# Kernel tuning notes

Hardware: AMD Instinct MI355X
Metric: run time of the kernel (lower is better)

## Reference

```python
import jax, jax.numpy as jnp
import numpy as np

D_MODEL = 768
N_HEADS = 12
HEAD_DIM = D_MODEL // N_HEADS
D_FF = 3072
LN_EPS = 1e-12


def layer_norm(x, gamma, beta, eps=LN_EPS):
    mu = jnp.mean(x, axis=-1, keepdims=True)
    var = jnp.var(x, axis=-1, keepdims=True)
    return (x - mu) * jax.lax.rsqrt(var + eps) * gamma + beta


def setup_inputs() -> dict:
    key = jax.random.key(0)
    ks = jax.random.split(key, 16)
    B, S = 4, 2048
    p = lambda k, shape: (jax.random.normal(k, shape, dtype=jnp.float32) * 0.02)
    return {
        "hidden_states": jax.random.normal(ks[0], (B, S, D_MODEL), dtype=jnp.float32),
        "Wq": p(ks[1], (D_MODEL, D_MODEL)), "bq": jnp.zeros((D_MODEL,), jnp.float32),
        "Wk": p(ks[2], (D_MODEL, D_MODEL)), "bk": jnp.zeros((D_MODEL,), jnp.float32),
        "Wv": p(ks[3], (D_MODEL, D_MODEL)), "bv": jnp.zeros((D_MODEL,), jnp.float32),
        "Wo": p(ks[4], (D_MODEL, D_MODEL)), "bo": jnp.zeros((D_MODEL,), jnp.float32),
        "ln1_g": jnp.ones((D_MODEL,), jnp.float32), "ln1_b": jnp.zeros((D_MODEL,), jnp.float32),
        "Wi": p(ks[5], (D_FF, D_MODEL)), "bi": jnp.zeros((D_FF,), jnp.float32),
        "Wf": p(ks[6], (D_MODEL, D_FF)), "bf": jnp.zeros((D_MODEL,), jnp.float32),
        "ln2_g": jnp.ones((D_MODEL,), jnp.float32), "ln2_b": jnp.zeros((D_MODEL,), jnp.float32),
    }


def reference(hidden_states, Wq, bq, Wk, bk, Wv, bv, Wo, bo, ln1_g, ln1_b,
              Wi, bi, Wf, bf, ln2_g, ln2_b):
    B, S, _ = hidden_states.shape
    # Q/K/V projections (computed as in source; outputs then overwritten by constants)
    q = hidden_states @ Wq.T + bq
    k = hidden_states @ Wk.T + bk
    v = hidden_states @ Wv.T + bv
    split = lambda x: x.reshape(B, S, N_HEADS, HEAD_DIM).transpose(0, 2, 1, 3)
    q, k, v = split(q), split(k), split(v)
    # source: torch.full_like(..., 0.01) overwrite of q/k/v
    q = jnp.full_like(q, 0.01)
    k = jnp.full_like(k, 0.01)
    v = jnp.full_like(v, 0.01)
    # naive attention: full [B,H,S,S] score matrix materialized
    scores = jnp.einsum("bhqd,bhkd->bhqk", q, k) / jnp.sqrt(jnp.float32(HEAD_DIM))
    probs = jax.nn.softmax(scores, axis=-1)
    ctx = jnp.einsum("bhqk,bhkd->bhqd", probs, v)
    ctx = ctx.transpose(0, 2, 1, 3).reshape(B, S, D_MODEL)
    # self-output: dense + residual + LayerNorm (dropout is identity in eval)
    attn_out = layer_norm(ctx @ Wo.T + bo + hidden_states, ln1_g, ln1_b)
    # FFN: fc1 + exact GELU, fc2 + residual + LayerNorm
    h = jax.nn.gelu(attn_out @ Wi.T + bi, approximate=False)
    layer_out = layer_norm(h @ Wf.T + bf + attn_out, ln2_g, ln2_b)
    return layer_out
```

## Files before the change

kernel.cpp:

```cpp
#include <hip/hip_runtime.h>
#include <hip/hip_bf16.h>
#include <cstdint>
#include <cstddef>


typedef __bf16 bf16;
typedef __attribute__((ext_vector_type(8))) __bf16 bf16x8;
typedef __attribute__((ext_vector_type(4))) __bf16 bf16x4;
typedef __attribute__((ext_vector_type(16))) float floatx16;

#define DM    768
#define DF    3072
#define MROWS 8192

#define N8          (DF * DM / 8)
#define CONV_BLOCKS (2 * N8 / 256)
#define CVEC_BLOCKS (DM / 4)

__device__ __forceinline__ void gl2lds16(const void* gp, void* lp) {
  __builtin_amdgcn_global_load_lds(
      (__attribute__((address_space(1))) void*)(void*)gp,
      (__attribute__((address_space(3))) void*)lp,
      16, 0, 0);
}

__device__ __forceinline__ float gelu_fast(float x) {
  float x2 = x * x;
  float m  = x * __builtin_fmaf(-0.1029641f, x2, -2.3025851f);
  float e  = __builtin_amdgcn_exp2f(m);
  return x * __builtin_amdgcn_rcpf(1.0f + e);
}

__global__ __launch_bounds__(256)
void prep_kernel(const float* __restrict__ Wi, const float* __restrict__ Wf,
                 bf16* __restrict__ Wib, bf16* __restrict__ Wfb,
                 const float* __restrict__ Wo, const float* __restrict__ bo,
                 float* __restrict__ cvec) {
  if (blockIdx.x < CONV_BLOCKS) {
    int i = blockIdx.x * 256 + threadIdx.x;
    const float* src = (i < N8) ? Wi : Wf;
    bf16* dst        = (i < N8) ? Wib : Wfb;
    int k            = (i < N8) ? i : i - N8;
    const float4* p = (const float4*)(src + (size_t)k * 8);
    float4 x = p[0], y = p[1];
    bf16x8 o;
    o[0]=(bf16)x.x; o[1]=(bf16)x.y; o[2]=(bf16)x.z; o[3]=(bf16)x.w;
    o[4]=(bf16)y.x; o[5]=(bf16)y.y; o[6]=(bf16)y.z; o[7]=(bf16)y.w;
    *(bf16x8*)(dst + (size_t)k * 8) = o;
  } else {
    int row  = (blockIdx.x - CONV_BLOCKS) * 4 + (threadIdx.x >> 6);
    int lane = threadIdx.x & 63;
    const float4* r = (const float4*)(Wo + (size_t)row * DM);
    float s = 0.f;
    #pragma unroll
    for (int t = 0; t < 3; ++t) {
      float4 v = r[lane + t * 64];
      s += v.x + v.y + v.z + v.w;
    }
    #pragma unroll
    for (int o = 32; o > 0; o >>= 1) s += __shfl_xor(s, o);
    if (lane == 0) cvec[row] = 0.01f * s + bo[row];
  }
}

__global__ __launch_bounds__(256)
void ln1_kernel(const float* __restrict__ hid, const float* __restrict__ cvec,
                const float* __restrict__ g, const float* __restrict__ b,
                bf16* __restrict__ out) {
  int row  = blockIdx.x * 4 + (threadIdx.x >> 6);
  int lane = threadIdx.x & 63;
  const float4* hrow = (const float4*)(hid + (size_t)row * DM);
  const float4* cv4  = (const float4*)cvec;
  float x[12];
  float s = 0.f, sq = 0.f;
  #pragma unroll
  for (int t = 0; t < 3; ++t) {
    int c = lane + t * 64;
    float4 v = hrow[c];
    float4 cc = cv4[c];
    float x0 = v.x + cc.x, x1 = v.y + cc.y, x2 = v.z + cc.z, x3 = v.w + cc.w;
    x[t*4+0] = x0; x[t*4+1] = x1; x[t*4+2] = x2; x[t*4+3] = x3;
    s  += x0 + x1 + x2 + x3;
    sq += x0*x0 + x1*x1 + x2*x2 + x3*x3;
  }
  #pragma unroll
  for (int o = 32; o > 0; o >>= 1) { s += __shfl_xor(s, o); sq += __shfl_xor(sq, o); }
  float mu  = s * (1.0f / DM);
  float var = sq * (1.0f / DM) - mu * mu;
  float inv = rsqrtf(var + 1e-12f);
  const float4* g4 = (const float4*)g;
  const float4* b4 = (const float4*)b;
  #pragma unroll
  for (int t = 0; t < 3; ++t) {
    int c = lane + t * 64;
    float4 gg = g4[c], bb = b4[c];
    bf16x4 o4;
    o4[0] = (bf16)((x[t*4+0] - mu) * inv * gg.x + bb.x);
    o4[1] = (bf16)((x[t*4+1] - mu) * inv * gg.y + bb.y);
    o4[2] = (bf16)((x[t*4+2] - mu) * inv * gg.z + bb.z);
    o4[3] = (bf16)((x[t*4+3] - mu) * inv * gg.w + bb.w);
    *(bf16x4*)(out + (size_t)row * DM + c * 4) = o4;
  }
}

__global__ __launch_bounds__(256)
void ln2_kernel(const bf16* __restrict__ p0, const bf16* __restrict__ p1,
                const float* __restrict__ bias, const bf16* __restrict__ attn,
                const float* __restrict__ g, const float* __restrict__ b,
                float* __restrict__ out) {
  int row  = blockIdx.x * 4 + (threadIdx.x >> 6);
  int lane = threadIdx.x & 63;
  const bf16* r0 = p0 + (size_t)row * DM;
  const bf16* r1 = p1 + (size_t)row * DM;
  const bf16* ar = attn + (size_t)row * DM;
  const float4* bi4 = (const float4*)bias;
  float x[12];
  float s = 0.f, sq = 0.f;
  #pragma unroll
  for (int t = 0; t < 3; ++t) {
    int c = lane + t * 64;
    bf16x4 a = *(const bf16x4*)(r0 + c * 4);
    bf16x4 d = *(const bf16x4*)(r1 + c * 4);
    bf16x4 rv = *(const bf16x4*)(ar + c * 4);
    float4 bb = bi4[c];
    float x0 = (float)a[0] + (float)d[0] + bb.x + (float)rv[0];
    float x1 = (float)a[1] + (float)d[1] + bb.y + (float)rv[1];
    float x2 = (float)a[2] + (float)d[2] + bb.z + (float)rv[2];
    float x3 = (float)a[3] + (float)d[3] + bb.w + (float)rv[3];
    x[t*4+0] = x0; x[t*4+1] = x1; x[t*4+2] = x2; x[t*4+3] = x3;
    s  += x0 + x1 + x2 + x3;
    sq += x0*x0 + x1*x1 + x2*x2 + x3*x3;
  }
  #pragma unroll
  for (int o = 32; o > 0; o >>= 1) { s += __shfl_xor(s, o); sq += __shfl_xor(sq, o); }
  float mu  = s * (1.0f / DM);
  float var = sq * (1.0f / DM) - mu * mu;
  float inv = rsqrtf(var + 1e-12f);
  const float4* g4 = (const float4*)g;
  const float4* b4 = (const float4*)b;
  float4* orow = (float4*)(out + (size_t)row * DM);
  #pragma unroll
  for (int t = 0; t < 3; ++t) {
    int c = lane + t * 64;
    float4 gg = g4[c], bb = b4[c];
    float4 o;
    o.x = (x[t*4+0] - mu) * inv * gg.x + bb.x;
    o.y = (x[t*4+1] - mu) * inv * gg.y + bb.y;
    o.z = (x[t*4+2] - mu) * inv * gg.z + bb.z;
    o.w = (x[t*4+3] - mu) * inv * gg.w + bb.w;
    orow[c] = o;
  }
}

#define BM 128
#define BN 128
#define BK 64
#define ES 136

template <int EPI>
__global__ __launch_bounds__(256)
void gemm_nt(const bf16* __restrict__ A, const bf16* __restrict__ B,
             const float* __restrict__ bias,
             bf16* __restrict__ out, int M, int N, int K, int ksplit, int NB) {
  __shared__ __align__(16) unsigned char smem[BM * ES * 2];
  bf16* lds_a = (bf16*)smem;
  bf16* lds_b = lds_a + BM * BK;

  const int tid   = threadIdx.x;
  const int wave  = tid >> 6;
  const int lane  = tid & 63;
  const int l31   = lane & 31;
  const int lhi   = lane >> 5;
  const int xorv  = lane & 7;

  const int ygrp = blockIdx.x;
  const int xz   = blockIdx.y;
  const int xb   = xz % NB;
  const int zb   = xz / NB;

  const int m0 = ygrp * BM;
  const int n0 = xb * BN;
  const int wm = (wave >> 1) * 64;
  const int wn = (wave & 1) * 64;

  const int kbeg = zb * ksplit;
  const int kend = kbeg + ksplit;

  floatx16 acc[2][2] = {};
  const bf16* Ablk = A + (size_t)m0 * K;
  const bf16* Bblk = B + (size_t)n0 * K;

  for (int kk = kbeg; kk < kend; kk += BK) {
    #pragma unroll
    for (int i = 0; i < 4; ++i) {
      int ci  = tid + 256 * i;
      int r   = ci >> 3;
      int c_g = (ci & 7) ^ (r & 7);
      gl2lds16(Ablk + (size_t)r * K + kk + c_g * 8, lds_a + ci * 8);
      gl2lds16(Bblk + (size_t)r * K + kk + c_g * 8, lds_b + ci * 8);
    }
    __syncthreads();

    #pragma unroll
    for (int ks = 0; ks < BK; ks += 16) {
      const int cs = ((ks >> 3) + lhi) ^ xorv;
      bf16x8 af[2], bfr[2];
      #pragma unroll
      for (int i = 0; i < 2; ++i)
        af[i] = *(const bf16x8*)&lds_a[(wm + i * 32 + l31) * BK + cs * 8];
      #pragma unroll
      for (int j = 0; j < 2; ++j)
        bfr[j] = *(const bf16x8*)&lds_b[(wn + j * 32 + l31) * BK + cs * 8];
      #pragma unroll
      for (int i = 0; i < 2; ++i)
        #pragma unroll
        for (int j = 0; j < 2; ++j)
          acc[i][j] = __builtin_amdgcn_mfma_f32_32x32x16_bf16(af[i], bfr[j], acc[i][j], 0, 0, 0);
    }
    __syncthreads();
  }

  bf16* eb = (bf16*)smem;

  float bia[2];
  if constexpr (EPI == 0) {
    #pragma unroll
    for (int j = 0; j < 2; ++j) bia[j] = bias[n0 + wn + j * 32 + l31];
  }

  #pragma unroll
  for (int i = 0; i < 2; ++i) {
    #pragma unroll
    for (int j = 0; j < 2; ++j) {
      int col = wn + j * 32 + l31;
      #pragma unroll
      for (int r = 0; r < 16; ++r) {
        int row = wm + i * 32 + (r & 3) + 8 * (r >> 2) + 4 * lhi;
        float x = acc[i][j][r];
        if constexpr (EPI == 0) x = gelu_fast(x + bia[j]);
        eb[row * ES + col] = (bf16)x;
      }
    }
  }
  __syncthreads();

  bf16* outp = out + (EPI == 1 ? (size_t)zb * M * N : 0);
  const int rsub = tid >> 4;
  const int csub = (tid & 15) * 8;
  #pragma unroll
  for (int c = 0; c < 8; ++c) {
    int row = c * 16 + rsub;
    bf16x8 v = *(const bf16x8*)&eb[row * ES + csub];
    *(bf16x8*)&outp[(size_t)(m0 + row) * N + n0 + csub] = v;
  }
}

extern "C" void kernel_launch(void* const* d_in, const int* in_sizes, int n_in,
                              void* d_out, int out_size, void* d_ws, size_t ws_size,
                              hipStream_t stream) {
  (void)in_sizes; (void)n_in; (void)out_size; (void)ws_size;

  const float* hidden = (const float*)d_in[0];
  const float* Wo     = (const float*)d_in[7];
  const float* bo     = (const float*)d_in[8];
  const float* ln1_g  = (const float*)d_in[9];
  const float* ln1_b  = (const float*)d_in[10];
  const float* Wi     = (const float*)d_in[11];
  const float* bi     = (const float*)d_in[12];
  const float* Wf     = (const float*)d_in[13];
  const float* bf_    = (const float*)d_in[14];
  const float* ln2_g  = (const float*)d_in[15];
  const float* ln2_b  = (const float*)d_in[16];
  float* out = (float*)d_out;

  char* w = (char*)d_ws;
  float* cvec = (float*)w;
  size_t off = 4096;
  bf16* attn = (bf16*)(w + off); off += (size_t)MROWS * DM * 2;
  bf16* h    = (bf16*)(w + off); off += (size_t)MROWS * DF * 2;
  bf16* pre  = (bf16*)(w + off); off += (size_t)2 * MROWS * DM * 2;
  bf16* Wib  = (bf16*)(w + off); off += (size_t)DF * DM * 2;
  bf16* Wfb  = (bf16*)(w + off);

  prep_kernel<<<dim3(CONV_BLOCKS + CVEC_BLOCKS), dim3(256), 0, stream>>>(
      Wi, Wf, Wib, Wfb, Wo, bo, cvec);

  ln1_kernel<<<dim3(MROWS / 4), dim3(256), 0, stream>>>(hidden, cvec, ln1_g, ln1_b, attn);

  gemm_nt<0><<<dim3(MROWS / BM, DF / BN), dim3(256), 0, stream>>>(
      attn, Wib, bi, h, MROWS, DF, DM, DM, DF / BN);

  gemm_nt<1><<<dim3(MROWS / BM, (DM / BN) * 2), dim3(256), 0, stream>>>(
      h, Wfb, nullptr, pre, MROWS, DM, DF, DF / 2, DM / BN);

  ln2_kernel<<<dim3(MROWS / 4), dim3(256), 0, stream>>>(
      pre, pre + (size_t)MROWS * DM, bf_, attn, ln2_g, ln2_b, out);
}
```

Before: 225.2 us.

## Replace GEMM with 256x256-tile 8-wave multi-stage pipelined MFMA kernel

Replaces the 128x128 single-buffered GEMM with a 256x256-tile, 512-thread kernel. It uses a 4-slot LDS ring filled by direct global-to-LDS loads that are issued ahead of compute, with explicit waitcnt and barrier scheduling and raised priority around the 16x16x32 MFMA blocks. Workgroups are remapped across XCDs for L2 locality, and the epilogue writes directly from registers, dropping the LDS staging. The goal is to hide memory latency and raise data reuse, at the cost of 128KB of LDS per block, heavy register use, and only 192 blocks for the second GEMM.

After: 243.3 us. +8.0%, slower.

```diff
diff --git a/kernel.cpp b/kernel.cpp
--- a/kernel.cpp
+++ b/kernel.cpp
@@ -7,7 +7,7 @@
 typedef __bf16 bf16;
 typedef __attribute__((ext_vector_type(8))) __bf16 bf16x8;
 typedef __attribute__((ext_vector_type(4))) __bf16 bf16x4;
-typedef __attribute__((ext_vector_type(16))) float floatx16;
+typedef __attribute__((ext_vector_type(4))) float  floatx4;
 
 #define DM    768
 #define DF    3072
@@ -152,106 +152,148 @@
   }
 }
 
-#define BM 128
-#define BN 128
-#define BK 64
-#define ES 136
-
 template <int EPI>
-__global__ __launch_bounds__(256)
-void gemm_nt(const bf16* __restrict__ A, const bf16* __restrict__ B,
-             const float* __restrict__ bias,
-             bf16* __restrict__ out, int M, int N, int K, int ksplit, int NB) {
-  __shared__ __align__(16) unsigned char smem[BM * ES * 2];
-  bf16* lds_a = (bf16*)smem;
-  bf16* lds_b = lds_a + BM * BK;
-
-  const int tid   = threadIdx.x;
-  const int wave  = tid >> 6;
-  const int lane  = tid & 63;
-  const int l31   = lane & 31;
-  const int lhi   = lane >> 5;
-  const int xorv  = lane & 7;
-
-  const int ygrp = blockIdx.x;
-  const int xz   = blockIdx.y;
-  const int xb   = xz % NB;
-  const int zb   = xz / NB;
-
-  const int m0 = ygrp * BM;
-  const int n0 = xb * BN;
-  const int wm = (wave >> 1) * 64;
-  const int wn = (wave & 1) * 64;
-
-  const int kbeg = zb * ksplit;
-  const int kend = kbeg + ksplit;
-
-  floatx16 acc[2][2] = {};
-  const bf16* Ablk = A + (size_t)m0 * K;
-  const bf16* Bblk = B + (size_t)n0 * K;
-
-  for (int kk = kbeg; kk < kend; kk += BK) {
-    #pragma unroll
-    for (int i = 0; i < 4; ++i) {
-      int ci  = tid + 256 * i;
-      int r   = ci >> 3;
-      int c_g = (ci & 7) ^ (r & 7);
-      gl2lds16(Ablk + (size_t)r * K + kk + c_g * 8, lds_a + ci * 8);
-      gl2lds16(Bblk + (size_t)r * K + kk + c_g * 8, lds_b + ci * 8);
+__global__ __launch_bounds__(512, 2)
+void gemm8p(const bf16* __restrict__ A, const bf16* __restrict__ B,
+            const float* __restrict__ bias, bf16* __restrict__ out,
+            int M, int N, int K, int ksplit, int NB, int CPX) {
+  extern __shared__ char smem[];
+
+  const int tid  = threadIdx.x;
+  const int lane = tid & 63;
+  const int wid  = tid >> 6;
+  const int wm   = (wid >> 2) * 128;
+  const int wn   = (wid & 3) * 64;
+  const int l15  = lane & 15;
+  const int kg   = lane >> 4;
+
+  const int wg = ((int)blockIdx.x & 7) * CPX + ((int)blockIdx.x >> 3);
+  int mb, nb, zb;
+  if constexpr (EPI == 0) { mb = wg / NB; nb = wg % NB; zb = 0; }
+  else { mb = wg / (2 * NB); int r = wg % (2 * NB); nb = r % NB; zb = r / NB; }
+
+  const int m0 = mb * 256, n0 = nb * 256;
+  const int NT = ksplit >> 6;
+  const bf16* Ab = A + (size_t)m0 * K + (size_t)zb * ksplit;
+  const bf16* Bb = B + (size_t)n0 * K + (size_t)zb * ksplit;
+
+  const int r0s = tid >> 2;
+  const int r1s = 128 + (tid >> 2);
+  const int kgp = tid & 3;
+  const int sw0 = (kgp ^ ((r0s >> 1) & 3)) << 3;
+  const int sw1 = (kgp ^ ((r1s >> 1) & 3)) << 3;
+  const int d0  = tid * 16;
+  const int d1  = (512 + tid) * 16;
+
+  auto stage = [&](int c) {
+    if (c >= 4 * NT) return;
+    const int tc = c >> 2, p = c & 3, ks = p >> 1, isB = p & 1;
+    const int slot = (2 * tc + ks) & 3;
+    char* base = smem + (isB ? 65536 : 0) + slot * 16384;
+    const bf16* src = isB ? Bb : Ab;
+    const int gk = tc * 64 + ks * 32;
+    gl2lds16(src + (size_t)r0s * K + gk + sw0, base + d0);
+    gl2lds16(src + (size_t)r1s * K + gk + sw1, base + d1);
+  };
+
+  int offA[8], offB[4];
+  #pragma unroll
+  for (int mf = 0; mf < 8; ++mf) {
+    int r = wm + mf * 16 + l15;
+    offA[mf] = r * 64 + ((kg ^ ((r >> 1) & 3)) << 4);
+  }
+  #pragma unroll
+  for (int nf = 0; nf < 4; ++nf) {
+    int r = wn + nf * 16 + l15;
+    offB[nf] = 65536 + r * 64 + ((kg ^ ((r >> 1) & 3)) << 4);
+  }
+
+  floatx4 acc[8][4] = {};
+
+  #pragma unroll
+  for (int c = 0; c < 6; ++c) stage(c);
+  asm volatile("s_waitcnt vmcnt(4)" ::: "memory");
+  __builtin_amdgcn_s_barrier();
+
+  for (int t = 0; t < NT; ++t) {
+    const int s2t = 2 * t;
+    #pragma unroll
+    for (int ks = 0; ks < 2; ++ks) {
+      const int slot = (s2t + ks) & 3;
+      char* sbase = smem + slot * 16384;
+
+      bf16x8 af[4], bq[4];
+      #pragma unroll
+      for (int i = 0; i < 4; ++i) af[i] = *(const bf16x8*)(sbase + offA[i]);
+      #pragma unroll
+      for (int j = 0; j < 4; ++j) bq[j] = *(const bf16x8*)(sbase + offB[j]);
+      stage(4 * t + 2 * ks + 6);
+      __builtin_amdgcn_s_barrier();
+      asm volatile("s_waitcnt lgkmcnt(0)" ::: "memory");
+      __builtin_amdgcn_sched_barrier(0);
+      __builtin_amdgcn_s_setprio(1);
+      #pragma unroll
+      for (int i = 0; i < 4; ++i)
+        #pragma unroll
+        for (int j = 0; j < 4; ++j)
+          acc[i][j] = __builtin_amdgcn_mfma_f32_16x16x32_bf16(
+              bq[j], af[i], acc[i][j], 0, 0, 0);
+      __builtin_amdgcn_s_setprio(0);
+      __builtin_amdgcn_s_barrier();
+
+      #pragma unroll
+      for (int i = 0; i < 4; ++i) af[i] = *(const bf16x8*)(sbase + offA[4 + i]);
+      stage(4 * t + 2 * ks + 7);
+      __builtin_amdgcn_s_barrier();
+      asm volatile("s_waitcnt lgkmcnt(0)" ::: "memory");
+      __builtin_amdgcn_sched_barrier(0);
+      __builtin_amdgcn_s_setprio(1);
+      #pragma unroll
+      for (int i = 0; i < 4; ++i)
+        #pragma unroll
+        for (int j = 0; j < 4; ++j)
+          acc[4 + i][j] = __builtin_amdgcn_mfma_f32_16x16x32_bf16(
+              bq[j], af[i], acc[4 + i][j], 0, 0, 0);
+      __builtin_amdgcn_s_setprio(0);
+      if (ks == 1) {
+        if (t < NT - 2) { asm volatile("s_waitcnt vmcnt(4)" ::: "memory"); }
+        else            { asm volatile("s_waitcnt vmcnt(0)" ::: "memory"); }
+      }
+      __builtin_amdgcn_s_barrier();
     }
-    __syncthreads();
-
-    #pragma unroll
-    for (int ks = 0; ks < BK; ks += 16) {
-      const int cs = ((ks >> 3) + lhi) ^ xorv;
-      bf16x8 af[2], bfr[2];
-      #pragma unroll
-      for (int i = 0; i < 2; ++i)
-        af[i] = *(const bf16x8*)&lds_a[(wm + i * 32 + l31) * BK + cs * 8];
-      #pragma unroll
-      for (int j = 0; j < 2; ++j)
-        bfr[j] = *(const bf16x8*)&lds_b[(wn + j * 32 + l31) * BK + cs * 8];
-      #pragma unroll
-      for (int i = 0; i < 2; ++i)
-        #pragma unroll
-        for (int j = 0; j < 2; ++j)
-          acc[i][j] = __builtin_amdgcn_mfma_f32_32x32x16_bf16(af[i], bfr[j], acc[i][j], 0, 0, 0);
-    }
-    __syncthreads();
-  }
-
-  bf16* eb = (bf16*)smem;
-
-  float bia[2];
+  }
+
   if constexpr (EPI == 0) {
-    #pragma unroll
-    for (int j = 0; j < 2; ++j) bia[j] = bias[n0 + wn + j * 32 + l31];
-  }
-
-  #pragma unroll
-  for (int i = 0; i < 2; ++i) {
-    #pragma unroll
-    for (int j = 0; j < 2; ++j) {
-      int col = wn + j * 32 + l31;
-      #pragma unroll
-      for (int r = 0; r < 16; ++r) {
-        int row = wm + i * 32 + (r & 3) + 8 * (r >> 2) + 4 * lhi;
-        float x = acc[i][j][r];
-        if constexpr (EPI == 0) x = gelu_fast(x + bia[j]);
-        eb[row * ES + col] = (bf16)x;
+    float4 bb[4];
+    #pragma unroll
+    for (int nf = 0; nf < 4; ++nf)
+      bb[nf] = *(const float4*)(bias + n0 + wn + nf * 16 + kg * 4);
+    #pragma unroll
+    for (int mf = 0; mf < 8; ++mf) {
+      bf16* orow = out + (size_t)(m0 + wm + mf * 16 + l15) * N + n0 + wn + kg * 4;
+      #pragma unroll
+      for (int nf = 0; nf < 4; ++nf) {
+        bf16x4 o;
+        o[0] = (bf16)gelu_fast(acc[mf][nf][0] + bb[nf].x);
+        o[1] = (bf16)gelu_fast(acc[mf][nf][1] + bb[nf].y);
+        o[2] = (bf16)gelu_fast(acc[mf][nf][2] + bb[nf].z);
+        o[3] = (bf16)gelu_fast(acc[mf][nf][3] + bb[nf].w);
+        *(bf16x4*)(orow + nf * 16) = o;
       }
     }
-  }
-  __syncthreads();
-
-  bf16* outp = out + (EPI == 1 ? (size_t)zb * M * N : 0);
-  const int rsub = tid >> 4;
-  const int csub = (tid & 15) * 8;
-  #pragma unroll
-  for (int c = 0; c < 8; ++c) {
-    int row = c * 16 + rsub;
-    bf16x8 v = *(const bf16x8*)&eb[row * ES + csub];
-    *(bf16x8*)&outp[(size_t)(m0 + row) * N + n0 + csub] = v;
+  } else {
+    bf16* op = out + (size_t)zb * M * N;
+    #pragma unroll
+    for (int mf = 0; mf < 8; ++mf) {
+      bf16* orow = op + (size_t)(m0 + wm + mf * 16 + l15) * N + n0 + wn + kg * 4;
+      #pragma unroll
+      for (int nf = 0; nf < 4; ++nf) {
+        bf16x4 o;
+        #pragma unroll
+        for (int q = 0; q < 4; ++q) o[q] = (bf16)acc[mf][nf][q];
+        *(bf16x4*)(orow + nf * 16) = o;
+      }
+    }
   }
 }
 
@@ -282,16 +324,25 @@
   bf16* Wib  = (bf16*)(w + off); off += (size_t)DF * DM * 2;
   bf16* Wfb  = (bf16*)(w + off);
 
+  static bool attr_done = false;
+  if (!attr_done) {
+    (void)hipFuncSetAttribute(reinterpret_cast<const void*>(&gemm8p<0>),
+        hipFuncAttributeMaxDynamicSharedMemorySize, 131072);
+    (void)hipFuncSetAttribute(reinterpret_cast<const void*>(&gemm8p<1>),
+        hipFuncAttributeMaxDynamicSharedMemorySize, 131072);
+    attr_done = true;
+  }
+
   prep_kernel<<<dim3(CONV_BLOCKS + CVEC_BLOCKS), dim3(256), 0, stream>>>(
       Wi, Wf, Wib, Wfb, Wo, bo, cvec);
 
   ln1_kernel<<<dim3(MROWS / 4), dim3(256), 0, stream>>>(hidden, cvec, ln1_g, ln1_b, attn);
 
-  gemm_nt<0><<<dim3(MROWS / BM, DF / BN), dim3(256), 0, stream>>>(
-      attn, Wib, bi, h, MROWS, DF, DM, DM, DF / BN);
-
-  gemm_nt<1><<<dim3(MROWS / BM, (DM / BN) * 2), dim3(256), 0, stream>>>(
-      h, Wfb, nullptr, pre, MROWS, DM, DF, DF / 2, DM / BN);
+  gemm8p<0><<<dim3(384), dim3(512), 131072, stream>>>(
+      attn, Wib, bi, h, MROWS, DF, DM, DM, DF / 256, 384 / 8);
+
+  gemm8p<1><<<dim3(192), dim3(512), 131072, stream>>>(
+      h, Wfb, nullptr, pre, MROWS, DM, DF, DF / 2, DM / 256, 192 / 8);
 
   ln2_kernel<<<dim3(MROWS / 4), dim3(256), 0, stream>>>(
       pre, pre + (size_t)MROWS * DM, bf_, attn, ln2_g, ln2_b, out);
```

## Double-buffer GEMM LDS tiles and swap MFMA operands for vectorized epilogue stores

Applied to the files above, without the earlier changes.

The GEMM main loop now uses two 32KB LDS buffers, issuing global-to-LDS loads for the next K tile while MFMAs run on the current one, and drops one barrier per iteration. The MFMA operands are swapped so each lane holds four consecutive output columns. This lets the epilogue write bf16x4 vectors to LDS and load the bias as a float4 instead of issuing scalar stores. LDS use grows to 64KB per block, which may reduce occupancy.

Measured after the change: 224.6 us. About the same (-0.2%).

```diff
diff --git a/kernel.cpp b/kernel.cpp
--- a/kernel.cpp
+++ b/kernel.cpp
@@ -162,9 +162,7 @@
 void gemm_nt(const bf16* __restrict__ A, const bf16* __restrict__ B,
              const float* __restrict__ bias,
              bf16* __restrict__ out, int M, int N, int K, int ksplit, int NB) {
-  __shared__ __align__(16) unsigned char smem[BM * ES * 2];
-  bf16* lds_a = (bf16*)smem;
-  bf16* lds_b = lds_a + BM * BK;
+  __shared__ __align__(16) unsigned char smem[65536];
 
   const int tid   = threadIdx.x;
   const int wave  = tid >> 6;
@@ -184,61 +182,78 @@
   const int wn = (wave & 1) * 64;
 
   const int kbeg = zb * ksplit;
-  const int kend = kbeg + ksplit;
+  const int NT   = ksplit / BK;
 
   floatx16 acc[2][2] = {};
   const bf16* Ablk = A + (size_t)m0 * K;
   const bf16* Bblk = B + (size_t)n0 * K;
 
-  for (int kk = kbeg; kk < kend; kk += BK) {
+  auto stage = [&](int bf, int kk) {
+    bf16* la = (bf16*)(smem + bf * 32768);
+    bf16* lb = la + BM * BK;
     #pragma unroll
     for (int i = 0; i < 4; ++i) {
       int ci  = tid + 256 * i;
       int r   = ci >> 3;
       int c_g = (ci & 7) ^ (r & 7);
-      gl2lds16(Ablk + (size_t)r * K + kk + c_g * 8, lds_a + ci * 8);
-      gl2lds16(Bblk + (size_t)r * K + kk + c_g * 8, lds_b + ci * 8);
+      gl2lds16(Ablk + (size_t)r * K + kk + c_g * 8, la + ci * 8);
+      gl2lds16(Bblk + (size_t)r * K + kk + c_g * 8, lb + ci * 8);
     }
+  };
+
+  stage(0, kbeg);
+  int buf = 0;
+  for (int t = 0; t < NT; ++t) {
     __syncthreads();
-
+    if (t + 1 < NT) stage(buf ^ 1, kbeg + (t + 1) * BK);
+    const bf16* la = (const bf16*)(smem + buf * 32768);
+    const bf16* lb = la + BM * BK;
     #pragma unroll
     for (int ks = 0; ks < BK; ks += 16) {
       const int cs = ((ks >> 3) + lhi) ^ xorv;
       bf16x8 af[2], bfr[2];
       #pragma unroll
       for (int i = 0; i < 2; ++i)
-        af[i] = *(const bf16x8*)&lds_a[(wm + i * 32 + l31) * BK + cs * 8];
+        af[i] = *(const bf16x8*)&la[(wm + i * 32 + l31) * BK + cs * 8];
       #pragma unroll
       for (int j = 0; j < 2; ++j)
-        bfr[j] = *(const bf16x8*)&lds_b[(wn + j * 32 + l31) * BK + cs * 8];
+        bfr[j] = *(const bf16x8*)&lb[(wn + j * 32 + l31) * BK + cs * 8];
       #pragma unroll
       for (int i = 0; i < 2; ++i)
         #pragma unroll
         for (int j = 0; j < 2; ++j)
-          acc[i][j] = __builtin_amdgcn_mfma_f32_32x32x16_bf16(af[i], bfr[j], acc[i][j], 0, 0, 0);
+          acc[i][j] = __builtin_amdgcn_mfma_f32_32x32x16_bf16(
+              bfr[j], af[i], acc[i][j], 0, 0, 0);
     }
-    __syncthreads();
-  }
+    buf ^= 1;
+  }
+  __syncthreads();
 
   bf16* eb = (bf16*)smem;
 
-  float bia[2];
-  if constexpr (EPI == 0) {
-    #pragma unroll
-    for (int j = 0; j < 2; ++j) bia[j] = bias[n0 + wn + j * 32 + l31];
-  }
-
   #pragma unroll
   for (int i = 0; i < 2; ++i) {
     #pragma unroll
     for (int j = 0; j < 2; ++j) {
-      int col = wn + j * 32 + l31;
+      const int rowb = wm + i * 32 + l31;
+      const int colb = wn + j * 32 + 4 * lhi;
       #pragma unroll
-      for (int r = 0; r < 16; ++r) {
-        int row = wm + i * 32 + (r & 3) + 8 * (r >> 2) + 4 * lhi;
-        float x = acc[i][j][r];
-        if constexpr (EPI == 0) x = gelu_fast(x + bia[j]);
-        eb[row * ES + col] = (bf16)x;
+      for (int rq = 0; rq < 4; ++rq) {
+        const int col = colb + rq * 8;
+        bf16x4 o;
+        if constexpr (EPI == 0) {
+          float4 bb = *(const float4*)(bias + n0 + col);
+          o[0] = (bf16)gelu_fast(acc[i][j][rq*4+0] + bb.x);
+          o[1] = (bf16)gelu_fast(acc[i][j][rq*4+1] + bb.y);
+          o[2] = (bf16)gelu_fast(acc[i][j][rq*4+2] + bb.z);
+          o[3] = (bf16)gelu_fast(acc[i][j][rq*4+3] + bb.w);
+        } else {
+          o[0] = (bf16)acc[i][j][rq*4+0];
+          o[1] = (bf16)acc[i][j][rq*4+1];
+          o[2] = (bf16)acc[i][j][rq*4+2];
+          o[3] = (bf16)acc[i][j][rq*4+3];
+        }
+        *(bf16x4*)&eb[rowb * ES + col] = o;
       }
     }
   }
```
